# Optimization experiments

Measured on AMD Instinct MI355X. Metric: run time of the kernel, lower is better.

## Reference

```python
import jax, jax.numpy as jnp
import numpy as np

MIN_LEVEL, MAX_LEVEL = 2, 5

# pywt Wavelet('db4') analysis filters (dec_lo / dec_hi)
DEC_LO = np.array([-0.010597401784997278, 0.032883011666982945, 0.030841381835986965,
                   -0.18703481171888114, -0.02798376941698385, 0.6308807679295904,
                   0.7148465705525415, 0.23037781330885523])
DEC_HI = np.array([-0.23037781330885523, 0.7148465705525415, -0.6308807679295904,
                   -0.02798376941698385, 0.18703481171888114, 0.030841381835986965,
                   -0.032883011666982945, -0.010597401784997278])
# pytorch_wavelets time-reverses the filters and uses cross-correlation (F.conv),
# which is exactly what lax.conv_general_dilated computes.
H0 = jnp.asarray(DEC_LO[::-1].copy(), jnp.float32)
H1 = jnp.asarray(DEC_HI[::-1].copy(), jnp.float32)


def _afb1d(x):
    """One-level analysis filter bank, 'zero' padding mode (pytorch_wavelets afb1d).
    x: (N, 1, T) -> (lo, hi) each (N, 1, floor((T+L-1)/2))."""
    T = x.shape[-1]
    L = H0.shape[0]
    out = (T + L - 1) // 2          # pywt.dwt_coeff_len(T, L, 'zero')
    p = 2 * out - T                 # total pad; extra zero goes to the right if odd
    xp = jnp.pad(x, ((0, 0), (0, 0), (p // 2, p - p // 2)))
    k = jnp.stack([H0, H1])[:, None, :]          # (2, 1, L)
    lohi = jax.lax.conv_general_dilated(
        xp, k, window_strides=(2,), padding='VALID',
        dimension_numbers=('NCH', 'OIH', 'NCH'))
    return lohi[:, 0:1, :], lohi[:, 1:2, :]


def _decompose(x, levels):
    """Batched multi-level DWT cascade over all features at once; per-feature
    decomposition level selected afterwards via one-hot / masking (same math as
    the original per-feature Python loop)."""
    B, S, F = x.shape
    cur = jnp.transpose(x, (0, 2, 1)).reshape(B * F, 1, S)
    los, his = [], []
    for _ in range(MAX_LEVEL):
        lo, hi = _afb1d(cur)

        def to_bsf(a):
            # zero-pad coeffs up to seq_len, back to (B, S, F) layout
            a = jnp.pad(a, ((0, 0), (0, 0), (0, S - a.shape[-1])))
            return jnp.transpose(a.reshape(B, F, S), (0, 2, 1))

        los.append(to_bsf(lo))
        his.append(to_bsf(hi))
        cur = lo
    los = jnp.stack(los)   # (MAX_LEVEL, B, S, F) lowpass after level j+1
    his = jnp.stack(his)   # (MAX_LEVEL, B, S, F) detail at level j+1

    # approx for feature f = lowpass after `levels[f]` levels
    sel = jax.nn.one_hot(levels - 1, MAX_LEVEL, dtype=x.dtype)      # (F, MAX_LEVEL)
    approx = jnp.einsum('lbsf,fl->bsf', los, sel)
    # details[i] only populated for i < levels[f]
    mask = (jnp.arange(MAX_LEVEL)[:, None] < levels[None, :]).astype(x.dtype)  # (L, F)
    details = his * mask[:, None, None, :]
    high_freq = details.sum(axis=0)
    low_freq = approx
    return approx, details, high_freq, low_freq


def setup_inputs() -> dict:
    key = jax.random.key(0)
    k1, k2 = jax.random.split(key)
    x = jax.random.normal(k1, (32, 4096, 64), jnp.float32)
    complexity_scores = jax.random.uniform(k2, (64,), jnp.float32)
    return {"x": x, "complexity_scores": complexity_scores}


def reference(x, complexity_scores):
    # level_scaled = min_level + round(score * (max_level - min_level)); Python round
    # and jnp.round both use round-half-to-even.
    levels = MIN_LEVEL + jnp.round(
        complexity_scores * (MAX_LEVEL - MIN_LEVEL)).astype(jnp.int32)
    levels = jnp.clip(levels, MIN_LEVEL, MAX_LEVEL)   # (F,)
    return _decompose(x, levels)
```

## Files before the change

### kernel.cpp

```cpp
#include <hip/hip_runtime.h>


#define NB 32
#define NS 4096
#define NF 64
#define BSF (NB * NS * NF)
#define NF4 (NF / 4)

typedef float f4v __attribute__((ext_vector_type(4)));

__constant__ float c_h0[8] = {
     0.23037781330885523f,  0.7148465705525415f,   0.6308807679295904f,
    -0.02798376941698385f, -0.18703481171888114f,  0.030841381835986965f,
     0.032883011666982945f, -0.010597401784997278f};
__constant__ float c_h1[8] = {
    -0.010597401784997278f, -0.032883011666982945f, 0.030841381835986965f,
     0.18703481171888114f,  -0.02798376941698385f,  -0.6308807679295904f,
     0.7148465705525415f,   -0.23037781330885523f};

__device__ __forceinline__ int get_level(const float* __restrict__ scores, int f) {
    int lv = 2 + (int)rintf(scores[f] * 3.0f);
    return min(5, max(2, lv));
}

template <int J, int TIN, int LOG2LEN>
__global__ __launch_bounds__(256) void wl_lvl(
    const f4v* __restrict__ in, f4v* __restrict__ lo_out,
    f4v* __restrict__ det, const float* __restrict__ scores)
{
    constexpr int LEN = 1 << LOG2LEN;
    int t = blockIdx.x * 256 + threadIdx.x;
    int f4 = t & (NF4 - 1);
    int r = t >> 4;
    int np = r & (LEN / 2 - 1);
    int b = r >> (LOG2LEN - 1);
    int n0 = 2 * np;

    const f4v* row = in + (size_t)b * TIN * NF4 + f4;
    const f4v z = {0.f, 0.f, 0.f, 0.f};
    f4v v[10];
    int base = n0 * 2 - 3;
#pragma unroll
    for (int j = 0; j < 10; ++j) {
        int m = base + j;
        v[j] = ((unsigned)m < (unsigned)TIN) ? row[(size_t)m * NF4] : z;
    }
    f4v lo0 = z, hi0 = z, lo1 = z, hi1 = z;
#pragma unroll
    for (int i = 0; i < 8; ++i) {
        lo0 += c_h0[i] * v[i];      hi0 += c_h1[i] * v[i];
        lo1 += c_h0[i] * v[i + 2];  hi1 += c_h1[i] * v[i + 2];
    }
    if (J >= 3) {
        int f0 = f4 * 4;
#pragma unroll
        for (int c = 0; c < 4; ++c)
            if (get_level(scores, f0 + c) < J) { hi0[c] = 0.f; hi1[c] = 0.f; }
    }
    f4v* lp = lo_out + (size_t)(b * LEN + n0) * NF4 + f4;
    lp[0] = lo0;  lp[NF4] = lo1;
    f4v* dp = det + (size_t)(b * NS + n0) * NF4 + f4;
    dp[0] = hi0;  dp[NF4] = hi1;
}

__global__ __launch_bounds__(256) void wl_final(
    const float* __restrict__ lo2s, const float* __restrict__ lo3s,
    const float* __restrict__ lo4s, f4v* __restrict__ out4,
    const float* __restrict__ scores)
{
    int t = blockIdx.x * 256 + threadIdx.x;
    int f4 = t & (NF4 - 1);
    int r = t >> 4;
    int n = r & (NS - 1);
    int b = r >> 12;
    int f0 = f4 * 4;

    int lv[4];
#pragma unroll
    for (int c = 0; c < 4; ++c) lv[c] = get_level(scores, f0 + c);

    const f4v z = {0.f, 0.f, 0.f, 0.f};
    f4v d5 = z, l5 = z;
    if (n < 128) {
        const f4v* row = (const f4v*)lo4s + (size_t)b * 256 * NF4 + f4;
        int base = 2 * n - 3;
        f4v hi = z;
#pragma unroll
        for (int i = 0; i < 8; ++i) {
            int m = base + i;
            if ((unsigned)m < 256u) {
                f4v v = row[(size_t)m * NF4];
                l5 += c_h0[i] * v;  hi += c_h1[i] * v;
            }
        }
#pragma unroll
        for (int c = 0; c < 4; ++c) d5[c] = (lv[c] >= 5) ? hi[c] : 0.f;
    }

    f4v* det1 = out4 + (size_t)1 * (BSF / 4);
    f4v* det2 = out4 + (size_t)2 * (BSF / 4);
    f4v* det3 = out4 + (size_t)3 * (BSF / 4);
    f4v* det4 = out4 + (size_t)4 * (BSF / 4);

    f4v acc = d5;
    if (n < 2048) {
        acc += det1[t];
        if (n < 1024) acc += det2[t];
        if (n < 512)  acc += det3[t];
        if (n < 256)  acc += det4[t];
    }

    f4v av = z;
#pragma unroll
    for (int c = 0; c < 4; ++c) {
        int L = lv[c];
        int len = 2048 >> (L - 1);
        float vv = 0.f;
        if (n < len) {
            if (L == 5)      vv = l5[c];
            else if (L == 4) vv = lo4s[(size_t)(b * 256 + n) * NF + f0 + c];
            else if (L == 3) vv = lo3s[(size_t)(b * 512 + n) * NF + f0 + c];
            else             vv = lo2s[(size_t)(b * 1024 + n) * NF + f0 + c];
        }
        av[c] = vv;
    }

    __builtin_nontemporal_store(av,  out4 + t);
    __builtin_nontemporal_store(d5,  out4 + (size_t)5 * (BSF / 4) + t);
    __builtin_nontemporal_store(acc, out4 + (size_t)6 * (BSF / 4) + t);
    __builtin_nontemporal_store(av,  out4 + (size_t)7 * (BSF / 4) + t);
    if (n >= 2048) __builtin_nontemporal_store(z, det1 + t);
    if (n >= 1024) __builtin_nontemporal_store(z, det2 + t);
    if (n >= 512)  __builtin_nontemporal_store(z, det3 + t);
    if (n >= 256)  __builtin_nontemporal_store(z, det4 + t);
}

extern "C" void kernel_launch(void* const* d_in, const int* in_sizes, int n_in,
                              void* d_out, int out_size, void* d_ws, size_t ws_size,
                              hipStream_t stream)
{
    const f4v* x        = (const f4v*)d_in[0];
    const float* scores = (const float*)d_in[1];
    f4v* out4 = (f4v*)d_out;
    float* ws = (float*)d_ws;

    f4v* lo1 = (f4v*)ws;
    f4v* lo2 = lo1 + (size_t)NB * 2048 * NF4;
    f4v* lo3 = lo2 + (size_t)NB * 1024 * NF4;
    f4v* lo4 = lo3 + (size_t)NB * 512 * NF4;

    f4v* det1 = out4 + (size_t)1 * (BSF / 4);
    f4v* det2 = out4 + (size_t)2 * (BSF / 4);
    f4v* det3 = out4 + (size_t)3 * (BSF / 4);
    f4v* det4 = out4 + (size_t)4 * (BSF / 4);

    dim3 block(256);
    wl_lvl<1, 4096, 11><<<dim3(NB * 1024 * NF4 / 256), block, 0, stream>>>(x,   lo1, det1, scores);
    wl_lvl<2, 2048, 10><<<dim3(NB *  512 * NF4 / 256), block, 0, stream>>>(lo1, lo2, det2, scores);
    wl_lvl<3, 1024,  9><<<dim3(NB *  256 * NF4 / 256), block, 0, stream>>>(lo2, lo3, det3, scores);
    wl_lvl<4,  512,  8><<<dim3(NB *  128 * NF4 / 256), block, 0, stream>>>(lo3, lo4, det4, scores);
    wl_final<<<dim3(BSF / 4 / 256), block, 0, stream>>>((const float*)lo2, (const float*)lo3,
                                                        (const float*)lo4, out4, scores);
}
```

Baseline: 308.4 us.

## Move zero-fill of detail tails into level kernels and split final kernel by output

Each level kernel now launches over the full sequence length. Threads past the level's output length write the zero tail of that detail buffer, so the final kernel no longer does it. Each thread computes one output position instead of two, which drops the shared-window register reuse. The final kernel is split into four regions (approx, approx copy, d5, high_freq), each thread writing one output, and the level-5 lowpass is computed only when some feature needs it. This spreads the store work over more threads but recomputes the level-5 filter in several regions and launches many idle-ish threads in the level kernels.

```diff
diff --git a/kernel.cpp b/kernel.cpp
--- a/kernel.cpp
+++ b/kernel.cpp
@@ -32,35 +32,37 @@
     int t = blockIdx.x * 256 + threadIdx.x;
     int f4 = t & (NF4 - 1);
     int r = t >> 4;
-    int np = r & (LEN / 2 - 1);
-    int b = r >> (LOG2LEN - 1);
-    int n0 = 2 * np;
+    int n = r & (NS - 1);
+    int b = r >> 12;
+
+    f4v* dp = det + (size_t)(b * NS + n) * NF4 + f4;
+    const f4v z = {0.f, 0.f, 0.f, 0.f};
+    if (n >= LEN) {
+        __builtin_nontemporal_store(z, dp);
+        return;
+    }
 
     const f4v* row = in + (size_t)b * TIN * NF4 + f4;
-    const f4v z = {0.f, 0.f, 0.f, 0.f};
-    f4v v[10];
-    int base = n0 * 2 - 3;
-#pragma unroll
-    for (int j = 0; j < 10; ++j) {
-        int m = base + j;
-        v[j] = ((unsigned)m < (unsigned)TIN) ? row[(size_t)m * NF4] : z;
-    }
-    f4v lo0 = z, hi0 = z, lo1 = z, hi1 = z;
+    int base = 2 * n - 3;
+    f4v lo = z, hi = z;
 #pragma unroll
     for (int i = 0; i < 8; ++i) {
-        lo0 += c_h0[i] * v[i];      hi0 += c_h1[i] * v[i];
-        lo1 += c_h0[i] * v[i + 2];  hi1 += c_h1[i] * v[i + 2];
+        int m = base + i;
+        if ((unsigned)m < (unsigned)TIN) {
+            f4v v = row[(size_t)m * NF4];
+            lo += c_h0[i] * v;
+            hi += c_h1[i] * v;
+        }
     }
     if (J >= 3) {
         int f0 = f4 * 4;
 #pragma unroll
         for (int c = 0; c < 4; ++c)
-            if (get_level(scores, f0 + c) < J) { hi0[c] = 0.f; hi1[c] = 0.f; }
+            if (get_level(scores, f0 + c) < J) hi[c] = 0.f;
     }
-    f4v* lp = lo_out + (size_t)(b * LEN + n0) * NF4 + f4;
-    lp[0] = lo0;  lp[NF4] = lo1;
-    f4v* dp = det + (size_t)(b * NS + n0) * NF4 + f4;
-    dp[0] = hi0;  dp[NF4] = hi1;
+    lo_out[(size_t)(b * LEN + n) * NF4 + f4] = lo;
+    dp[0] = hi;
+    (void)dp;
 }
 
 __global__ __launch_bounds__(256) void wl_final(
@@ -69,8 +71,10 @@
     const float* __restrict__ scores)
 {
     int t = blockIdx.x * 256 + threadIdx.x;
-    int f4 = t & (NF4 - 1);
-    int r = t >> 4;
+    int reg = t >> 21;
+    int idx = t & ((1 << 21) - 1);
+    int f4 = idx & (NF4 - 1);
+    int r = idx >> 4;
     int n = r & (NS - 1);
     int b = r >> 12;
     int f0 = f4 * 4;
@@ -80,59 +84,69 @@
     for (int c = 0; c < 4; ++c) lv[c] = get_level(scores, f0 + c);
 
     const f4v z = {0.f, 0.f, 0.f, 0.f};
-    f4v d5 = z, l5 = z;
-    if (n < 128) {
-        const f4v* row = (const f4v*)lo4s + (size_t)b * 256 * NF4 + f4;
-        int base = 2 * n - 3;
-        f4v hi = z;
-#pragma unroll
-        for (int i = 0; i < 8; ++i) {
-            int m = base + i;
-            if ((unsigned)m < 256u) {
-                f4v v = row[(size_t)m * NF4];
-                l5 += c_h0[i] * v;  hi += c_h1[i] * v;
-            }
-        }
-#pragma unroll
-        for (int c = 0; c < 4; ++c) d5[c] = (lv[c] >= 5) ? hi[c] : 0.f;
-    }
+    const f4v* lo4row = (const f4v*)lo4s + (size_t)b * 256 * NF4 + f4;
 
     f4v* det1 = out4 + (size_t)1 * (BSF / 4);
     f4v* det2 = out4 + (size_t)2 * (BSF / 4);
     f4v* det3 = out4 + (size_t)3 * (BSF / 4);
     f4v* det4 = out4 + (size_t)4 * (BSF / 4);
 
+    if (reg <= 1) {
+        f4v l5 = z;
+        if (n < 128 && (lv[0] == 5 || lv[1] == 5 || lv[2] == 5 || lv[3] == 5)) {
+            int base = 2 * n - 3;
+#pragma unroll
+            for (int i = 0; i < 8; ++i) {
+                int m = base + i;
+                if ((unsigned)m < 256u) l5 += c_h0[i] * lo4row[(size_t)m * NF4];
+            }
+        }
+        f4v av = z;
+#pragma unroll
+        for (int c = 0; c < 4; ++c) {
+            int L = lv[c];
+            int len = 2048 >> (L - 1);
+            float vv = 0.f;
+            if (n < len) {
+                if (L == 5)      vv = l5[c];
+                else if (L == 4) vv = lo4s[(size_t)(b * 256 + n) * NF + f0 + c];
+                else if (L == 3) vv = lo3s[(size_t)(b * 512 + n) * NF + f0 + c];
+                else             vv = lo2s[(size_t)(b * 1024 + n) * NF + f0 + c];
+            }
+            av[c] = vv;
+        }
+        f4v* dst = (reg == 0) ? (out4 + idx)
+                              : (out4 + (size_t)7 * (BSF / 4) + idx);
+        __builtin_nontemporal_store(av, dst);
+        return;
+    }
+
+    f4v d5 = z;
+    if (n < 128) {
+        int base = 2 * n - 3;
+        f4v hi = z;
+#pragma unroll
+        for (int i = 0; i < 8; ++i) {
+            int m = base + i;
+            if ((unsigned)m < 256u) hi += c_h1[i] * lo4row[(size_t)m * NF4];
+        }
+#pragma unroll
+        for (int c = 0; c < 4; ++c) d5[c] = (lv[c] >= 5) ? hi[c] : 0.f;
+    }
+
+    if (reg == 2) {
+        __builtin_nontemporal_store(d5, out4 + (size_t)5 * (BSF / 4) + idx);
+        return;
+    }
+
     f4v acc = d5;
     if (n < 2048) {
-        acc += det1[t];
-        if (n < 1024) acc += det2[t];
-        if (n < 512)  acc += det3[t];
-        if (n < 256)  acc += det4[t];
+        acc += det1[idx];
+        if (n < 1024) acc += det2[idx];
+        if (n < 512)  acc += det3[idx];
+        if (n < 256)  acc += det4[idx];
     }
-
-    f4v av = z;
-#pragma unroll
-    for (int c = 0; c < 4; ++c) {
-        int L = lv[c];
-        int len = 2048 >> (L - 1);
-        float vv = 0.f;
-        if (n < len) {
-            if (L == 5)      vv = l5[c];
-            else if (L == 4) vv = lo4s[(size_t)(b * 256 + n) * NF + f0 + c];
-            else if (L == 3) vv = lo3s[(size_t)(b * 512 + n) * NF + f0 + c];
-            else             vv = lo2s[(size_t)(b * 1024 + n) * NF + f0 + c];
-        }
-        av[c] = vv;
-    }
-
-    __builtin_nontemporal_store(av,  out4 + t);
-    __builtin_nontemporal_store(d5,  out4 + (size_t)5 * (BSF / 4) + t);
-    __builtin_nontemporal_store(acc, out4 + (size_t)6 * (BSF / 4) + t);
-    __builtin_nontemporal_store(av,  out4 + (size_t)7 * (BSF / 4) + t);
-    if (n >= 2048) __builtin_nontemporal_store(z, det1 + t);
-    if (n >= 1024) __builtin_nontemporal_store(z, det2 + t);
-    if (n >= 512)  __builtin_nontemporal_store(z, det3 + t);
-    if (n >= 256)  __builtin_nontemporal_store(z, det4 + t);
+    __builtin_nontemporal_store(acc, out4 + (size_t)6 * (BSF / 4) + idx);
 }
 
 extern "C" void kernel_launch(void* const* d_in, const int* in_sizes, int n_in,
@@ -155,10 +169,11 @@
     f4v* det4 = out4 + (size_t)4 * (BSF / 4);
 
     dim3 block(256);
-    wl_lvl<1, 4096, 11><<<dim3(NB * 1024 * NF4 / 256), block, 0, stream>>>(x,   lo1, det1, scores);
-    wl_lvl<2, 2048, 10><<<dim3(NB *  512 * NF4 / 256), block, 0, stream>>>(lo1, lo2, det2, scores);
-    wl_lvl<3, 1024,  9><<<dim3(NB *  256 * NF4 / 256), block, 0, stream>>>(lo2, lo3, det3, scores);
-    wl_lvl<4,  512,  8><<<dim3(NB *  128 * NF4 / 256), block, 0, stream>>>(lo3, lo4, det4, scores);
-    wl_final<<<dim3(BSF / 4 / 256), block, 0, stream>>>((const float*)lo2, (const float*)lo3,
-                                                        (const float*)lo4, out4, scores);
+    const int FULL = NB * NS * NF4 / 256;
+    wl_lvl<1, 4096, 11><<<dim3(FULL), block, 0, stream>>>(x,   lo1, det1, scores);
+    wl_lvl<2, 2048, 10><<<dim3(FULL), block, 0, stream>>>(lo1, lo2, det2, scores);
+    wl_lvl<3, 1024,  9><<<dim3(FULL), block, 0, stream>>>(lo2, lo3, det3, scores);
+    wl_lvl<4,  512,  8><<<dim3(FULL), block, 0, stream>>>(lo3, lo4, det4, scores);
+    wl_final<<<dim3(4 * FULL), block, 0, stream>>>((const float*)lo2, (const float*)lo3,
+                                                   (const float*)lo4, out4, scores);
 }
```

Measured after the change: 303.0 us. Within noise of the previous version (-1.7%).
